# Optimization experiments

Hardware: AMD Instinct MI355X
Metric: run time of the kernel (lower is better)

Reference implementation:

```python
import jax, jax.numpy as jnp
import numpy as np


def setup_inputs() -> dict:
    key = jax.random.key(0)
    k1, k2, k3 = jax.random.split(key, 3)
    B, F, D = 8192, 4096, 1024
    x = jax.random.normal(k1, (B, D), dtype=jnp.float32)
    mu = jax.random.normal(k2, (F, D), dtype=jnp.float32)
    # keep scales strictly positive and well-conditioned
    scale_diag = jax.random.uniform(k3, (F, D), dtype=jnp.float32, minval=0.5, maxval=1.5)
    return {"x": x, "mu": mu, "scale_diag": scale_diag}


def reference(x, mu, scale_diag):
    # Unnormalized diag-Gaussian log prob for every (batch, feature) pair:
    #   out[b, f] = sum_d -0.5 * ((x[b,d] - mu[f,d]) / scale[f,d])^2
    # Expanded to GEMM form (quadratic expansion):
    #   -0.5 * ( x^2 @ inv2.T  -  2 * x @ (mu*inv2).T  +  sum_d mu^2*inv2 )
    inv2 = 1.0 / (scale_diag * scale_diag)            # [F, D]
    xx = jnp.matmul(x * x, inv2.T)                    # [B, F]
    xm = jnp.matmul(x, (mu * inv2).T)                 # [B, F]
    mm = jnp.sum(mu * mu * inv2, axis=-1)             # [F]
    return -0.5 * (xx - 2.0 * xm + mm[None, :])       # [B, F]
```

## Files before the change

### kernel.cpp

```cpp
#include <hip/hip_runtime.h>
#include <hip/hip_bf16.h>
#include <cstdint>

#define B_SZ 8192
#define F_SZ 4096
#define D_SZ 1024
#define K_SZ 2048

typedef __bf16 bf16x8 __attribute__((ext_vector_type(8)));
typedef float f32x4 __attribute__((ext_vector_type(4)));
typedef float fvec4 __attribute__((ext_vector_type(4)));
typedef unsigned short u16x4 __attribute__((ext_vector_type(4)));

__device__ __forceinline__ unsigned short f2bf(float f) {
    union { float f; unsigned u; } c; c.f = f;
    unsigned r = c.u + 0x7fff + ((c.u >> 16) & 1);
    return (unsigned short)(r >> 16);
}

__device__ __forceinline__ void async16(const void* g, void* l) {
    __builtin_amdgcn_global_load_lds(
        (__attribute__((address_space(1))) void*)g,
        (__attribute__((address_space(3))) void*)l, 16, 0, 0);
}

__global__ __launch_bounds__(256) void prep(const float* __restrict__ x,
                                            const float* __restrict__ mu,
                                            const float* __restrict__ sd,
                                            unsigned short* __restrict__ A,
                                            unsigned short* __restrict__ W,
                                            float* __restrict__ nmm) {
    const int tid = threadIdx.x;
    if (blockIdx.x < 4096) {
        const size_t o0 = (size_t)blockIdx.x * 2048 + tid * 4;
        fvec4 v0 = *(const fvec4*)(x + o0);
        fvec4 v1 = *(const fvec4*)(x + o0 + 1024);
        #pragma unroll
        for (int h = 0; h < 2; ++h) {
            fvec4 v = h ? v1 : v0;
            size_t oo = o0 + h * 1024;
            size_t b = oo >> 10;
            int d = (int)(oo & 1023);
            u16x4 xx, xs;
            xx.x = f2bf(v.x * v.x); xx.y = f2bf(v.y * v.y);
            xx.z = f2bf(v.z * v.z); xx.w = f2bf(v.w * v.w);
            xs.x = f2bf(v.x); xs.y = f2bf(v.y);
            xs.z = f2bf(v.z); xs.w = f2bf(v.w);
            *(u16x4*)(A + b * K_SZ + d) = xx;
            *(u16x4*)(A + b * K_SZ + 1024 + d) = xs;
        }
    } else {
        const int f = blockIdx.x - 4096;
        const int d = tid * 4;
        size_t off = (size_t)f * D_SZ + d;
        fvec4 m = *(const fvec4*)(mu + off);
        fvec4 s = *(const fvec4*)(sd + off);
        float i0 = 1.0f / (s.x * s.x), i1 = 1.0f / (s.y * s.y);
        float i2 = 1.0f / (s.z * s.z), i3 = 1.0f / (s.w * s.w);
        u16x4 wi, wm;
        wi.x = f2bf(i0); wi.y = f2bf(i1); wi.z = f2bf(i2); wi.w = f2bf(i3);
        wm.x = f2bf(-2.0f * m.x * i0); wm.y = f2bf(-2.0f * m.y * i1);
        wm.z = f2bf(-2.0f * m.z * i2); wm.w = f2bf(-2.0f * m.w * i3);
        size_t wb = (size_t)f * K_SZ + d;
        *(u16x4*)(W + wb) = wi;
        *(u16x4*)(W + wb + 1024) = wm;
        float mm = m.x * m.x * i0 + m.y * m.y * i1 + m.z * m.z * i2 + m.w * m.w * i3;
        #pragma unroll
        for (int o = 32; o > 0; o >>= 1) mm += __shfl_down(mm, o, 64);
        __shared__ float red[4];
        if ((tid & 63) == 0) red[tid >> 6] = mm;
        __syncthreads();
        if (tid == 0) nmm[f] = -0.5f * (red[0] + red[1] + red[2] + red[3]);
    }
}

__global__ __launch_bounds__(512, 2) void gemm_bt(const unsigned short* __restrict__ A,
                                                  const unsigned short* __restrict__ W,
                                                  const float* __restrict__ nmm,
                                                  float* __restrict__ out) {
    __shared__ __align__(16) unsigned short sA[2][2][256 * 32];
    __shared__ __align__(16) unsigned short sB[2][2][256 * 32];

    const int tid  = threadIdx.x;
    const int wave = tid >> 6;
    const int lane = tid & 63;
    const int r16  = lane & 15;
    const int quad = lane >> 4;
    const int wmB  = (wave >> 2) * 128;
    const int wnB  = (wave & 3) * 64;
    const int tileM = blockIdx.y * 256;
    const int tileN = blockIdx.x * 256;

    const int srow   = tid >> 2;
    const int schunk = tid & 3;

    const f32x4 vzero = {0.f, 0.f, 0.f, 0.f};
    f32x4 acc[8][4];
    #pragma unroll
    for (int i = 0; i < 8; ++i)
        #pragma unroll
        for (int j = 0; j < 4; ++j) acc[i][j] = vzero;

    bf16x8 af[4], bfr[4];

#define BARW() __builtin_amdgcn_s_barrier()
#define VM4()  asm volatile("s_waitcnt vmcnt(4)" ::: "memory")
#define VM6()  asm volatile("s_waitcnt vmcnt(6)" ::: "memory")
#define VM0()  asm volatile("s_waitcnt vmcnt(0)" ::: "memory")

#define STAGE(S, G, TB, DB, KK, KT)                                          \
    { _Pragma("unroll")                                                      \
      for (int is_ = 0; is_ < 2; ++is_) {                                    \
          int rr_ = is_ * 128 + srow;                                        \
          int gc_ = ((schunk ^ ((rr_ >> 1) & 3)) << 3);                      \
          async16(G + (size_t)((TB) + rr_) * K_SZ + (KT) * 64 + (KK) * 32 + gc_, \
                  &S[DB][KK][0] + is_ * 4096 + wave * 512);                  \
      } }

#define READ_A(I0, DB, KK)                                                   \
    { _Pragma("unroll")                                                      \
      for (int i_ = 0; i_ < 4; ++i_) {                                       \
          int row_ = wmB + ((I0) + i_) * 16 + r16;                           \
          af[i_] = *(const bf16x8*)(&sA[DB][KK][0] + row_ * 32 +             \
                                    (((quad ^ (row_ >> 1)) & 3) << 3));      \
      } }

#define READ_B(DB, KK)                                                       \
    { _Pragma("unroll")                                                      \
      for (int j_ = 0; j_ < 4; ++j_) {                                       \
          int row_ = wnB + j_ * 16 + r16;                                    \
          bfr[j_] = *(const bf16x8*)(&sB[DB][KK][0] + row_ * 32 +            \
                                     (((quad ^ (row_ >> 1)) & 3) << 3));     \
      } }

#define MFMA16(I0)                                                           \
    __builtin_amdgcn_s_setprio(1);                                          \
    { _Pragma("unroll")                                                      \
      for (int i_ = 0; i_ < 4; ++i_)                                         \
          _Pragma("unroll")                                                  \
          for (int j_ = 0; j_ < 4; ++j_)                                     \
              acc[(I0) + i_][j_] = __builtin_amdgcn_mfma_f32_16x16x32_bf16(  \
                  af[i_], bfr[j_], acc[(I0) + i_][j_], 0, 0, 0); }           \
    __builtin_amdgcn_s_setprio(0);

#define PH(RB, I0, DB, KK, DOSTG, SBUF, G, TB, SDB, SKK, SKT, VM)            \
    { if (RB) READ_B(DB, KK)                                                 \
      READ_A(I0, DB, KK)                                                     \
      if (DOSTG) STAGE(SBUF, G, TB, SDB, SKK, SKT)                           \
      MFMA16(I0)                                                             \
      if ((VM) == 4) VM4(); else if ((VM) == 6) VM6(); else if ((VM) == 0) VM0(); \
      BARW(); }

#define ITER(T, S58)                                                         \
    PH(1, 0, 0, 0, 1,      sA, A, tileM, 1, 0, (T) + 1, -1)                  \
    PH(0, 4, 0, 0, 1,      sB, W, tileN, 1, 0, (T) + 1, -1)                  \
    PH(1, 0, 0, 1, 1,      sA, A, tileM, 1, 1, (T) + 1, -1)                  \
    PH(0, 4, 0, 1, 1,      sB, W, tileN, 1, 1, (T) + 1, 4)                   \
    PH(1, 0, 1, 0, (S58),  sA, A, tileM, 0, 0, (T) + 2, -1)                  \
    PH(0, 4, 1, 0, (S58),  sB, W, tileN, 0, 0, (T) + 2, (S58) ? -1 : 0)      \
    PH(1, 0, 1, 1, (S58),  sA, A, tileM, 0, 1, (T) + 2, -1)                  \
    PH(0, 4, 1, 1, (S58),  sB, W, tileN, 0, 1, (T) + 2, (S58) ? 6 : -1)

    STAGE(sA, A, tileM, 0, 0, 0)
    STAGE(sB, W, tileN, 0, 0, 0)
    STAGE(sA, A, tileM, 0, 1, 0)
    STAGE(sB, W, tileN, 0, 1, 0)
    VM4(); BARW();

    #pragma unroll 1
    for (int X = 0; X < 15; ++X) {
        const int T = 2 * X;
        ITER(T, 1)
    }
    {
        const int T = 30;
        ITER(T, 0)
    }

#undef PH
#undef ITER

    int   fc[4];
    float cj[4];
    #pragma unroll
    for (int j = 0; j < 4; ++j) {
        fc[j] = tileN + wnB + j * 16 + r16;
        cj[j] = nmm[fc[j]];
    }
    #pragma unroll
    for (int i = 0; i < 8; ++i) {
        int mbase = tileM + wmB + i * 16 + quad * 4;
        #pragma unroll
        for (int r = 0; r < 4; ++r) {
            float* orow = out + (size_t)(mbase + r) * F_SZ;
            #pragma unroll
            for (int j = 0; j < 4; ++j)
                orow[fc[j]] = -0.5f * acc[i][j][r] + cj[j];
        }
    }
}

extern "C" void kernel_launch(void* const* d_in, const int* in_sizes, int n_in,
                              void* d_out, int out_size, void* d_ws, size_t ws_size,
                              hipStream_t stream) {
    const float* x  = (const float*)d_in[0];
    const float* mu = (const float*)d_in[1];
    const float* sd = (const float*)d_in[2];
    float* out = (float*)d_out;

    unsigned short* A = (unsigned short*)d_ws;
    unsigned short* W = A + (size_t)B_SZ * K_SZ;
    float* nmm = (float*)(W + (size_t)F_SZ * K_SZ);

    prep<<<8192, 256, 0, stream>>>(x, mu, sd, A, W, nmm);
    gemm_bt<<<dim3(F_SZ / 256, B_SZ / 256), 512, 0, stream>>>(A, W, nmm, out);
}
```

Measured before the change: 300.1 us.

## Software-pipeline LDS fragment reads with double registers and swizzle block order

The GEMM main loop now double-buffers A/B fragments in registers, so the LDS reads for the next phase are issued before the current MFMA block runs, with fine-grained lgkmcnt waits and sched barriers. The grid is flattened to 1D and remapped so consecutive blocks share tiles, which improves L2 reuse. Global and LDS offsets are also precomputed to cut address arithmetic. The cost is higher register pressure from the extra fragment buffers, which may hurt occupancy at the 2-wave launch bound.

```diff
diff --git a/kernel.cpp b/kernel.cpp
--- a/kernel.cpp
+++ b/kernel.cpp
@@ -88,11 +88,33 @@
     const int quad = lane >> 4;
     const int wmB  = (wave >> 2) * 128;
     const int wnB  = (wave & 3) * 64;
-    const int tileM = blockIdx.y * 256;
-    const int tileN = blockIdx.x * 256;
+
+    const int id = blockIdx.x;
+    const int Ssw = ((id & 7) << 6) | (id >> 3);
+    const int xsw = Ssw >> 6, csw = Ssw & 63;
+    const int tileN = ((((xsw & 1) << 3) | (csw & 7))) << 8;
+    const int tileM = ((((xsw >> 1) << 3) | (csw >> 3))) << 8;
 
     const int srow   = tid >> 2;
     const int schunk = tid & 3;
+    const int gc = (schunk ^ ((srow >> 1) & 3)) << 3;
+    const unsigned short* gA0 = A + (size_t)(tileM + srow)       * K_SZ + gc;
+    const unsigned short* gA1 = A + (size_t)(tileM + 128 + srow) * K_SZ + gc;
+    const unsigned short* gW0 = W + (size_t)(tileN + srow)       * K_SZ + gc;
+    const unsigned short* gW1 = W + (size_t)(tileN + 128 + srow) * K_SZ + gc;
+    const int wdst = wave * 512;
+
+    int aOff[8], bOff[4];
+    #pragma unroll
+    for (int i = 0; i < 8; ++i) {
+        int row = wmB + i * 16 + r16;
+        aOff[i] = row * 64 + (((quad ^ (row >> 1)) & 3) << 4);
+    }
+    #pragma unroll
+    for (int j = 0; j < 4; ++j) {
+        int row = wnB + j * 16 + r16;
+        bOff[j] = row * 64 + (((quad ^ (row >> 1)) & 3) << 4);
+    }
 
     const f32x4 vzero = {0.f, 0.f, 0.f, 0.f};
     f32x4 acc[8][4];
@@ -101,83 +123,83 @@
         #pragma unroll
         for (int j = 0; j < 4; ++j) acc[i][j] = vzero;
 
-    bf16x8 af[4], bfr[4];
+    bf16x8 afA[4], afB[4], bfA[4], bfB[4];
 
 #define BARW() __builtin_amdgcn_s_barrier()
+#define SBAR() __builtin_amdgcn_sched_barrier(0)
+#define LGK4() asm volatile("s_waitcnt lgkmcnt(4)" ::: "memory")
+#define LGK8() asm volatile("s_waitcnt lgkmcnt(8)" ::: "memory")
+#define LGK0() asm volatile("s_waitcnt lgkmcnt(0)" ::: "memory")
 #define VM4()  asm volatile("s_waitcnt vmcnt(4)" ::: "memory")
-#define VM6()  asm volatile("s_waitcnt vmcnt(6)" ::: "memory")
 #define VM0()  asm volatile("s_waitcnt vmcnt(0)" ::: "memory")
 
-#define STAGE(S, G, TB, DB, KK, KT)                                          \
+#define STAGE4(DB, KK, KT)                                                   \
+    { const size_t ko_ = (size_t)((KT) * 64 + (KK) * 32);                    \
+      async16(gA0 + ko_, &sA[DB][KK][0] + wdst);                             \
+      async16(gA1 + ko_, &sA[DB][KK][0] + 4096 + wdst);                      \
+      async16(gW0 + ko_, &sB[DB][KK][0] + wdst);                             \
+      async16(gW1 + ko_, &sB[DB][KK][0] + 4096 + wdst); }
+
+#define RD_A4(DST, I0, DB, KK)                                               \
     { _Pragma("unroll")                                                      \
-      for (int is_ = 0; is_ < 2; ++is_) {                                    \
-          int rr_ = is_ * 128 + srow;                                        \
-          int gc_ = ((schunk ^ ((rr_ >> 1) & 3)) << 3);                      \
-          async16(G + (size_t)((TB) + rr_) * K_SZ + (KT) * 64 + (KK) * 32 + gc_, \
-                  &S[DB][KK][0] + is_ * 4096 + wave * 512);                  \
-      } }
-
-#define READ_A(I0, DB, KK)                                                   \
+      for (int i_ = 0; i_ < 4; ++i_)                                         \
+          DST[i_] = *(const bf16x8*)((const char*)&sA[DB][KK][0] +           \
+                                     aOff[(I0) + i_]); }
+
+#define RD_B4(DST, DB, KK)                                                   \
     { _Pragma("unroll")                                                      \
-      for (int i_ = 0; i_ < 4; ++i_) {                                       \
-          int row_ = wmB + ((I0) + i_) * 16 + r16;                           \
-          af[i_] = *(const bf16x8*)(&sA[DB][KK][0] + row_ * 32 +             \
-                                    (((quad ^ (row_ >> 1)) & 3) << 3));      \
-      } }
-
-#define READ_B(DB, KK)                                                       \
-    { _Pragma("unroll")                                                      \
-      for (int j_ = 0; j_ < 4; ++j_) {                                       \
-          int row_ = wnB + j_ * 16 + r16;                                    \
-          bfr[j_] = *(const bf16x8*)(&sB[DB][KK][0] + row_ * 32 +            \
-                                     (((quad ^ (row_ >> 1)) & 3) << 3));     \
-      } }
-
-#define MFMA16(I0)                                                           \
+      for (int j_ = 0; j_ < 4; ++j_)                                         \
+          DST[j_] = *(const bf16x8*)((const char*)&sB[DB][KK][0] +           \
+                                     bOff[j_]); }
+
+#define MM16(BF, AF, I0)                                                     \
     __builtin_amdgcn_s_setprio(1);                                          \
     { _Pragma("unroll")                                                      \
       for (int i_ = 0; i_ < 4; ++i_)                                         \
           _Pragma("unroll")                                                  \
           for (int j_ = 0; j_ < 4; ++j_)                                     \
               acc[(I0) + i_][j_] = __builtin_amdgcn_mfma_f32_16x16x32_bf16(  \
-                  af[i_], bfr[j_], acc[(I0) + i_][j_], 0, 0, 0); }           \
+                  AF[i_], BF[j_], acc[(I0) + i_][j_], 0, 0, 0); }            \
     __builtin_amdgcn_s_setprio(0);
 
-#define PH(RB, I0, DB, KK, DOSTG, SBUF, G, TB, SDB, SKK, SKT, VM)            \
-    { if (RB) READ_B(DB, KK)                                                 \
-      READ_A(I0, DB, KK)                                                     \
-      if (DOSTG) STAGE(SBUF, G, TB, SDB, SKK, SKT)                           \
-      MFMA16(I0)                                                             \
-      if ((VM) == 4) VM4(); else if ((VM) == 6) VM6(); else if ((VM) == 0) VM0(); \
-      BARW(); }
-
-#define ITER(T, S58)                                                         \
-    PH(1, 0, 0, 0, 1,      sA, A, tileM, 1, 0, (T) + 1, -1)                  \
-    PH(0, 4, 0, 0, 1,      sB, W, tileN, 1, 0, (T) + 1, -1)                  \
-    PH(1, 0, 0, 1, 1,      sA, A, tileM, 1, 1, (T) + 1, -1)                  \
-    PH(0, 4, 0, 1, 1,      sB, W, tileN, 1, 1, (T) + 1, 4)                   \
-    PH(1, 0, 1, 0, (S58),  sA, A, tileM, 0, 0, (T) + 2, -1)                  \
-    PH(0, 4, 1, 0, (S58),  sB, W, tileN, 0, 0, (T) + 2, (S58) ? -1 : 0)      \
-    PH(1, 0, 1, 1, (S58),  sA, A, tileM, 0, 1, (T) + 2, -1)                  \
-    PH(0, 4, 1, 1, (S58),  sB, W, tileN, 0, 1, (T) + 2, (S58) ? 6 : -1)
-
-    STAGE(sA, A, tileM, 0, 0, 0)
-    STAGE(sB, W, tileN, 0, 0, 0)
-    STAGE(sA, A, tileM, 0, 1, 0)
-    STAGE(sB, W, tileN, 0, 1, 0)
+#define ITER(T, LAST)                                                        \
+     RD_A4(afB, 4, 0, 0) STAGE4(1, 0, (T) + 1)                        \
+            SBAR(); LGK4(); SBAR(); MM16(bfA, afA, 0) VM4(); BARW();         \
+     RD_B4(bfB, 0, 1) RD_A4(afA, 0, 0, 1)                             \
+            SBAR(); LGK8(); SBAR(); MM16(bfA, afB, 4) BARW();                \
+     RD_A4(afB, 4, 0, 1) STAGE4(1, 1, (T) + 1)                        \
+            SBAR(); LGK4(); SBAR(); MM16(bfB, afA, 0) VM4(); BARW();         \
+     RD_B4(bfA, 1, 0) RD_A4(afA, 0, 1, 0)                             \
+            SBAR(); LGK8(); SBAR(); MM16(bfB, afB, 4) BARW();                \
+     RD_A4(afB, 4, 1, 0)                                              \
+            if (!(LAST)) { STAGE4(0, 0, (T) + 2) }                           \
+            SBAR(); LGK4(); SBAR(); MM16(bfA, afA, 0)                        \
+            if (LAST) { VM0(); } else { VM4(); } BARW();                     \
+     RD_B4(bfB, 1, 1) RD_A4(afA, 0, 1, 1)                             \
+            SBAR(); LGK8(); SBAR(); MM16(bfA, afB, 4) BARW();                \
+     RD_A4(afB, 4, 1, 1)                                              \
+            if (!(LAST)) { STAGE4(0, 1, (T) + 2) }                           \
+            SBAR(); LGK4(); SBAR(); MM16(bfB, afA, 0)                        \
+            if (!(LAST)) { VM4(); } BARW();                                  \
+     if (!(LAST)) { RD_B4(bfA, 0, 0) RD_A4(afA, 0, 0, 0) }            \
+            SBAR(); if (LAST) { LGK0(); } else { LGK8(); } SBAR();           \
+            MM16(bfB, afB, 4) BARW();
+
+    STAGE4(0, 0, 0)
+    STAGE4(0, 1, 0)
     VM4(); BARW();
+    RD_B4(bfA, 0, 0)
+    RD_A4(afA, 0, 0, 0)
 
     #pragma unroll 1
     for (int X = 0; X < 15; ++X) {
         const int T = 2 * X;
-        ITER(T, 1)
+        ITER(T, 0)
     }
     {
-        const int T = 30;
-        ITER(T, 0)
-    }
-
-#undef PH
+        ITER(30, 1)
+    }
+
 #undef ITER
 
     int   fc[4];
@@ -213,5 +235,5 @@
     float* nmm = (float*)(W + (size_t)F_SZ * K_SZ);
 
     prep<<<8192, 256, 0, stream>>>(x, mu, sd, A, W, nmm);
-    gemm_bt<<<dim3(F_SZ / 256, B_SZ / 256), 512, 0, stream>>>(A, W, nmm, out);
-}
+    gemm_bt<<<512, 512, 0, stream>>>(A, W, nmm, out);
+}
```

Measured after the change: 315.0 us. 5.0% more time.
